# Kernel tuning notes

Hardware: AMD Instinct MI355X
Metric: run time of the kernel (lower is better)

The kernel has to match this reference:

```python
import jax, jax.numpy as jnp
import numpy as np
from jax import lax

NUM_CLUSTER = 128
N_ITERS = 10


def setup_inputs() -> dict:
    key = jax.random.key(0)
    feat_g = jax.random.normal(key, (131072, 256), dtype=jnp.float32)
    return {"feat_g": feat_g}


def _sq_dists(x, c):
    x2 = jnp.sum(x * x, axis=1, keepdims=True)            # [N,1]
    c2 = jnp.sum(c * c, axis=1)                           # [K]
    return x2 - 2.0 * (x @ c.T) + c2[None, :]


def _kmeans_fit(x, k, iters):
    n = x.shape[0]
    init_c = x[:k]  # deterministic init: first k points
    ones = jnp.ones((n,), dtype=x.dtype)

    def step(c, _):
        assign = jnp.argmin(_sq_dists(x, c), axis=1)                 # [N]
        sums = jax.ops.segment_sum(x, assign, num_segments=k)       # [K,d]
        counts = jax.ops.segment_sum(ones, assign, num_segments=k)  # [K]
        new_c = sums / jnp.maximum(counts, 1.0)[:, None]
        new_c = jnp.where(counts[:, None] > 0, new_c, c)  # keep empty clusters
        return new_c, None

    c, _ = lax.scan(step, init_c, None, length=iters)
    return c


def reference(feat_g):
    # view(batch, -1, dim) then view(-1, dim) is an identity reshape for the math
    x = lax.stop_gradient(feat_g)  # original detaches feat_gc before fit/predict
    c = _kmeans_fit(x, NUM_CLUSTER, N_ITERS)
    preds = jnp.argmin(_sq_dists(x, c), axis=1)  # [N] int labels
    return preds
```

## Files before the change

### kernel.cpp

```cpp
#include <hip/hip_runtime.h>

#define NPTS 131072
#define DIM 256
#define NK 128
#define NITER 10
#define SEG 16
#define SLICES 128
#define PTS_PER_SLICE (NPTS / SLICES)
#define CHUNK 128

typedef _Float16 half8 __attribute__((ext_vector_type(8)));
typedef _Float16 half4v __attribute__((ext_vector_type(4)));
typedef float f32x4 __attribute__((ext_vector_type(4)));

#define RSCALE 4096.0f
#define RINV 2.44140625e-4f

__global__ void x2_kernel(const float* __restrict__ x, float* __restrict__ x2) {
  int tid = threadIdx.x;
  int p = blockIdx.x * 16 + (tid >> 4);
  int part = tid & 15;
  const float4* xr = (const float4*)(x + (size_t)p * DIM);
  float s = 0.f;
#pragma unroll
  for (int j = 0; j < 4; ++j) {
    float4 v = xr[part * 4 + j];
    s += v.x * v.x;
    s += v.y * v.y;
    s += v.z * v.z;
    s += v.w * v.w;
  }
#pragma unroll
  for (int m = 8; m >= 1; m >>= 1) s += __shfl_xor(s, m, 16);
  if (part == 0) x2[p] = s;
}

__global__ void c2_kernel(const float* __restrict__ c, float* __restrict__ c2) {
  int k = blockIdx.x, lane = threadIdx.x;
  float4 v = ((const float4*)(c + (size_t)k * DIM))[lane];
  float s = v.x * v.x + v.y * v.y + v.z * v.z + v.w * v.w;
#pragma unroll
  for (int m = 32; m >= 1; m >>= 1) s += __shfl_xor(s, m, 64);
  if (lane == 0) c2[k] = s;
}

__global__ void convert_x2_kernel(const float* __restrict__ x, _Float16* __restrict__ x1,
                                  _Float16* __restrict__ x2s, float* __restrict__ x2) {
  int tid = threadIdx.x;
  int p = blockIdx.x * 16 + (tid >> 4);
  int part = tid & 15;
  const float4* xr = (const float4*)(x + (size_t)p * DIM);
  half8* o1 = (half8*)(x1 + (size_t)p * DIM);
  half8* o2 = (half8*)(x2s + (size_t)p * DIM);
  float s = 0.f;
  half8 hh[2], ll[2];
#pragma unroll
  for (int j = 0; j < 4; ++j) {
    float4 v = xr[part * 4 + j];
    float f[4] = {v.x, v.y, v.z, v.w};
#pragma unroll
    for (int u = 0; u < 4; ++u) {
      _Float16 hi = (_Float16)f[u];
      float r = f[u] - (float)hi;
      hh[j >> 1][(j & 1) * 4 + u] = hi;
      ll[j >> 1][(j & 1) * 4 + u] = (_Float16)(r * RSCALE);
      s += f[u] * f[u];
    }
  }
#pragma unroll
  for (int jj = 0; jj < 2; ++jj) {
    o1[part * 2 + jj] = hh[jj];
    o2[part * 2 + jj] = ll[jj];
  }
#pragma unroll
  for (int m = 8; m >= 1; m >>= 1) s += __shfl_xor(s, m, 16);
  if (part == 0) x2[p] = s;
}

__global__ void convert_c_kernel(const float* __restrict__ c, _Float16* __restrict__ ct) {
  int i = blockIdx.x * 256 + threadIdx.x;
  int k = i >> 6;
  int d4 = i & 63;
  float4 v = ((const float4*)c)[i];
  float f[4] = {v.x, v.y, v.z, v.w};
  half4v h, l;
#pragma unroll
  for (int j = 0; j < 4; ++j) {
    _Float16 hi = (_Float16)f[j];
    float r = f[j] - (float)hi;
    h[j] = hi;
    l[j] = (_Float16)(r * RSCALE);
  }
  int ch = d4 >> 3;
  int idx4 = ch * 2048 + k * 8 + (d4 & 7);
  ((half4v*)ct)[idx4] = h;
  ((half4v*)ct)[idx4 + 1024] = l;
}

template <bool DOHIST>
__global__ __launch_bounds__(256, 2) void assign_mfma_kernel(
    const _Float16* __restrict__ x1, const _Float16* __restrict__ x2s,
    const _Float16* __restrict__ ct, const float* __restrict__ x2,
    const float* __restrict__ c2, int* __restrict__ out, int* __restrict__ counts) {
  __shared__ __align__(16) _Float16 cbuf[2][8192];
  __shared__ int hcnt[NK];

  int tid = threadIdx.x;
  int lane = tid & 63;
  int w = tid >> 6;
  int lcol = lane & 15;
  int lgrp = lane >> 4;
  int row0 = blockIdx.x * 128 + w * 32;

  if (DOHIST && tid < NK) hcnt[tid] = 0;

  const _Float16* xa = x1 + (size_t)(row0 + lcol) * DIM + lgrp * 8;
  const _Float16* xb = x2s + (size_t)(row0 + lcol) * DIM + lgrp * 8;
  const half8* ctv = (const half8*)ct;

  f32x4 acc1[2][8], acc2[2][8];
#pragma unroll
  for (int rt = 0; rt < 2; ++rt)
#pragma unroll
    for (int c8 = 0; c8 < 8; ++c8) {
      acc1[rt][c8] = f32x4{0.f, 0.f, 0.f, 0.f};
      acc2[rt][c8] = f32x4{0.f, 0.f, 0.f, 0.f};
    }

  half8 A1[2], A2[2], nA1[2], nA2[2];

#pragma unroll
  for (int r = 0; r < 4; ++r) {
    __builtin_amdgcn_global_load_lds(
        (const __attribute__((address_space(1))) void*)(ctv + r * 256 + tid),
        (__attribute__((address_space(3))) void*)&((half8*)cbuf[0])[r * 256 + tid], 16, 0, 0);
  }
#pragma unroll
  for (int rt = 0; rt < 2; ++rt) {
    A1[rt] = *(const half8*)(xa + rt * 16 * DIM);
    A2[rt] = *(const half8*)(xb + rt * 16 * DIM);
  }
  __syncthreads();

#pragma unroll
  for (int ck = 0; ck < 8; ++ck) {
    const int cb = ck & 1;
    if (ck < 7) {
#pragma unroll
      for (int r = 0; r < 4; ++r) {
        __builtin_amdgcn_global_load_lds(
            (const __attribute__((address_space(1))) void*)(ctv + (ck + 1) * 1024 + r * 256 + tid),
            (__attribute__((address_space(3))) void*)&((half8*)cbuf[cb ^ 1])[r * 256 + tid], 16, 0,
            0);
      }
#pragma unroll
      for (int rt = 0; rt < 2; ++rt) {
        nA1[rt] = *(const half8*)(xa + rt * 16 * DIM + (ck + 1) * 32);
        nA2[rt] = *(const half8*)(xb + rt * 16 * DIM + (ck + 1) * 32);
      }
    }
#pragma unroll
    for (int c8 = 0; c8 < 8; ++c8) {
      int bidx = (c8 * 16 + lcol) * 32 + lgrp * 8;
      half8 b1 = *(const half8*)&cbuf[cb][bidx];
      half8 b2 = *(const half8*)&cbuf[cb][4096 + bidx];
#pragma unroll
      for (int rt = 0; rt < 2; ++rt) {
        acc1[rt][c8] = __builtin_amdgcn_mfma_f32_16x16x32_f16(A1[rt], b1, acc1[rt][c8], 0, 0, 0);
        acc2[rt][c8] = __builtin_amdgcn_mfma_f32_16x16x32_f16(A1[rt], b2, acc2[rt][c8], 0, 0, 0);
        acc2[rt][c8] = __builtin_amdgcn_mfma_f32_16x16x32_f16(A2[rt], b1, acc2[rt][c8], 0, 0, 0);
      }
    }
    if (ck < 7) {
#pragma unroll
      for (int rt = 0; rt < 2; ++rt) {
        A1[rt] = nA1[rt];
        A2[rt] = nA2[rt];
      }
      __syncthreads();
    }
  }

#pragma unroll
  for (int rt = 0; rt < 2; ++rt) {
    int pbase = row0 + rt * 16 + lgrp * 4;
    float x2p[4];
#pragma unroll
    for (int r = 0; r < 4; ++r) x2p[r] = x2[pbase + r];
    float bv[4];
    int bk[4];
#pragma unroll
    for (int r = 0; r < 4; ++r) { bv[r] = 3.4e38f; bk[r] = 0; }
#pragma unroll
    for (int c8 = 0; c8 < 8; ++c8) {
      int kc = c8 * 16 + lcol;
      float c2k = c2[kc];
#pragma unroll
      for (int r = 0; r < 4; ++r) {
        float dot = fmaf(acc2[rt][c8][r], RINV, acc1[rt][c8][r]);
        float d = fmaf(-2.f, dot, x2p[r]) + c2k;
        if (d < bv[r]) { bv[r] = d; bk[r] = kc; }
      }
    }
#pragma unroll
    for (int m = 1; m <= 8; m <<= 1) {
#pragma unroll
      for (int r = 0; r < 4; ++r) {
        float ov = __shfl_xor(bv[r], m, 64);
        int ok = __shfl_xor(bk[r], m, 64);
        if (ov < bv[r] || (ov == bv[r] && ok < bk[r])) { bv[r] = ov; bk[r] = ok; }
      }
    }
    if (lcol == 0) {
#pragma unroll
      for (int r = 0; r < 4; ++r) {
        out[pbase + r] = bk[r];
        if (DOHIST) atomicAdd(&hcnt[bk[r]], 1);
      }
    }
  }

  if (DOHIST) {
    __syncthreads();
    if (tid < NK) {
      int v = hcnt[tid];
      if (v) atomicAdd(&counts[tid], v);
    }
  }
}

__global__ __launch_bounds__(256, 4) void csum_kernel(
    const _Float16* __restrict__ x1, const _Float16* __restrict__ x2s,
    const int* __restrict__ assignb, float* __restrict__ p) {
  __shared__ __align__(16) _Float16 bt[2][2][32][136];
  __shared__ int abuf[2][CHUNK];

  int tid = threadIdx.x;
  int lane = tid & 63;
  int w = tid >> 6;
  int slice = blockIdx.x;
  int d0 = blockIdx.y * 32;
  int ibase = slice * PTS_PER_SLICE;
  int kbase = w * 32;
  int lcol = lane & 15;
  int lgrp = lane >> 4;

  int sarr = tid >> 7;
  int srow = tid & 127;
  const _Float16* xsrc = sarr ? x2s : x1;

  f32x4 acc1[2][2], acc2[2][2];
#pragma unroll
  for (int kt = 0; kt < 2; ++kt)
#pragma unroll
    for (int dt = 0; dt < 2; ++dt) {
      acc1[kt][dt] = f32x4{0.f, 0.f, 0.f, 0.f};
      acc2[kt][dt] = f32x4{0.f, 0.f, 0.f, 0.f};
    }

  {
    const half8* src = (const half8*)(xsrc + (size_t)(ibase + srow) * DIM + d0);
    half8 v[4];
#pragma unroll
    for (int q = 0; q < 4; ++q) v[q] = src[q];
#pragma unroll
    for (int q = 0; q < 4; ++q)
#pragma unroll
      for (int j = 0; j < 8; ++j) bt[0][sarr][q * 8 + j][srow] = v[q][j];
    if (tid < 32) ((int4*)abuf[0])[tid] = ((const int4*)(assignb + ibase))[tid];
  }
  __syncthreads();

  const int NCH = PTS_PER_SLICE / CHUNK;
  for (int ci = 0; ci < NCH; ++ci) {
    const int cb = ci & 1;
    half8 nv[4];
    int4 na;
    bool more = (ci < NCH - 1);
    if (more) {
      const half8* src =
          (const half8*)(xsrc + (size_t)(ibase + (ci + 1) * CHUNK + srow) * DIM + d0);
#pragma unroll
      for (int q = 0; q < 4; ++q) nv[q] = src[q];
      if (tid < 32) na = ((const int4*)(assignb + ibase + (ci + 1) * CHUNK))[tid];
    }

#pragma unroll
    for (int ks = 0; ks < 4; ++ks) {
      int4 av0 = ((int4*)abuf[cb])[ks * 8 + lgrp * 2];
      int4 av1 = ((int4*)abuf[cb])[ks * 8 + lgrp * 2 + 1];
      int aj[8] = {av0.x, av0.y, av0.z, av0.w, av1.x, av1.y, av1.z, av1.w};
      half8 oh[2];
#pragma unroll
      for (int kt = 0; kt < 2; ++kt) {
        int kk = kbase + kt * 16 + lcol;
#pragma unroll
        for (int j = 0; j < 8; ++j) oh[kt][j] = (aj[j] == kk) ? (_Float16)1.0f : (_Float16)0.0f;
      }
#pragma unroll
      for (int dt = 0; dt < 2; ++dt) {
        half8 b1 = *(const half8*)&bt[cb][0][dt * 16 + lcol][ks * 32 + lgrp * 8];
        half8 b2 = *(const half8*)&bt[cb][1][dt * 16 + lcol][ks * 32 + lgrp * 8];
#pragma unroll
        for (int kt = 0; kt < 2; ++kt) {
          acc1[kt][dt] = __builtin_amdgcn_mfma_f32_16x16x32_f16(oh[kt], b1, acc1[kt][dt], 0, 0, 0);
          acc2[kt][dt] = __builtin_amdgcn_mfma_f32_16x16x32_f16(oh[kt], b2, acc2[kt][dt], 0, 0, 0);
        }
      }
    }

    if (more) {
      __syncthreads();
#pragma unroll
      for (int q = 0; q < 4; ++q)
#pragma unroll
        for (int j = 0; j < 8; ++j) bt[cb ^ 1][sarr][q * 8 + j][srow] = nv[q][j];
      if (tid < 32) ((int4*)abuf[cb ^ 1])[tid] = na;
      __syncthreads();
    }
  }

#pragma unroll
  for (int kt = 0; kt < 2; ++kt)
#pragma unroll
    for (int dt = 0; dt < 2; ++dt) {
      int dd = d0 + dt * 16 + lcol;
#pragma unroll
      for (int r = 0; r < 4; ++r) {
        int krow = kbase + kt * 16 + lgrp * 4 + r;
        p[((size_t)slice * NK + krow) * DIM + dd] = fmaf(acc2[kt][dt][r], RINV, acc1[kt][dt][r]);
      }
    }
}

__global__ void reduce_v4_kernel(const float* __restrict__ p, int* __restrict__ counts,
                                 float* __restrict__ c, float* __restrict__ c2,
                                 _Float16* __restrict__ ct) {
  __shared__ float wsum[4];
  int k = blockIdx.x, d = threadIdx.x;
  int cnt = counts[k];
  float s = 0.f;
#pragma unroll 8
  for (int sl = 0; sl < SLICES; ++sl) s += p[((size_t)sl * NK + k) * DIM + d];

  float nc;
  if (cnt > 0)
    nc = s / fmaxf((float)cnt, 1.0f);
  else
    nc = c[(size_t)k * DIM + d];
  c[(size_t)k * DIM + d] = nc;

  {
    _Float16 hi = (_Float16)nc;
    float r = nc - (float)hi;
    _Float16 lov = (_Float16)(r * RSCALE);
    int ch = d >> 5, dd = d & 31;
    ct[ch * 8192 + k * 32 + dd] = hi;
    ct[ch * 8192 + k * 32 + dd + 4096] = lov;
  }

  float sq = nc * nc;
#pragma unroll
  for (int m = 32; m >= 1; m >>= 1) sq += __shfl_xor(sq, m, 64);
  if ((threadIdx.x & 63) == 0) wsum[threadIdx.x >> 6] = sq;
  __syncthreads();
  if (threadIdx.x == 0) {
    c2[k] = wsum[0] + wsum[1] + wsum[2] + wsum[3];
    counts[k] = 0;
  }
}

__global__ void assign_kernel(const float* __restrict__ x, const float* __restrict__ c,
                              const float* __restrict__ x2, const float* __restrict__ c2,
                              int* __restrict__ assign_out) {
  __shared__ float4 xs4[64 * 4];
  __shared__ float4 cs4[128 * 4];
  __shared__ float redv[64][17];
  __shared__ int redk[64][17];

  int tid = threadIdx.x;
  int tx = tid & 15;
  int ty = tid >> 4;
  int row0 = blockIdx.x * 64;

  float acc[4][8];
#pragma unroll
  for (int a = 0; a < 4; ++a)
#pragma unroll
    for (int b = 0; b < 8; ++b) acc[a][b] = 0.f;

  for (int ck = 0; ck < 16; ++ck) {
    {
      int p = tid >> 2, d4 = tid & 3;
      float4 v = *(const float4*)(x + (size_t)(row0 + p) * DIM + ck * 16 + d4 * 4);
      xs4[p * 4 + (d4 ^ ((p >> 2) & 3))] = v;
    }
#pragma unroll
    for (int r = 0; r < 2; ++r) {
      int idx = tid + r * 256;
      int kk = idx >> 2, dd = idx & 3;
      float4 v = *(const float4*)(c + (size_t)kk * DIM + ck * 16 + dd * 4);
      cs4[kk * 4 + (dd ^ ((kk >> 3) & 3))] = v;
    }
    __syncthreads();
#pragma unroll
    for (int d4 = 0; d4 < 4; ++d4) {
      float4 xr[4], cr[8];
#pragma unroll
      for (int pp = 0; pp < 4; ++pp) xr[pp] = xs4[(tx * 4 + pp) * 4 + (d4 ^ (tx & 3))];
#pragma unroll
      for (int kk = 0; kk < 8; ++kk) cr[kk] = cs4[(ty * 8 + kk) * 4 + (d4 ^ (ty & 3))];
#pragma unroll
      for (int pp = 0; pp < 4; ++pp)
#pragma unroll
        for (int kk = 0; kk < 8; ++kk) {
          acc[pp][kk] = fmaf(xr[pp].x, cr[kk].x, acc[pp][kk]);
          acc[pp][kk] = fmaf(xr[pp].y, cr[kk].y, acc[pp][kk]);
          acc[pp][kk] = fmaf(xr[pp].z, cr[kk].z, acc[pp][kk]);
          acc[pp][kk] = fmaf(xr[pp].w, cr[kk].w, acc[pp][kk]);
        }
    }
    __syncthreads();
  }

  float x2p[4];
#pragma unroll
  for (int pp = 0; pp < 4; ++pp) x2p[pp] = x2[row0 + tx * 4 + pp];

  float bestv[4];
  int bestk[4];
#pragma unroll
  for (int pp = 0; pp < 4; ++pp) { bestv[pp] = 3.4e38f; bestk[pp] = 0; }
#pragma unroll
  for (int kk = 0; kk < 8; ++kk) {
    float c2k = c2[ty * 8 + kk];
#pragma unroll
    for (int pp = 0; pp < 4; ++pp) {
      float d = fmaf(-2.f, acc[pp][kk], x2p[pp]) + c2k;
      if (d < bestv[pp]) { bestv[pp] = d; bestk[pp] = ty * 8 + kk; }
    }
  }
#pragma unroll
  for (int pp = 0; pp < 4; ++pp) {
    redv[tx * 4 + pp][ty] = bestv[pp];
    redk[tx * 4 + pp][ty] = bestk[pp];
  }
  __syncthreads();
  if (tid < 64) {
    float bv = redv[tid][0];
    int bk = redk[tid][0];
#pragma unroll
    for (int t = 1; t < 16; ++t) {
      float v = redv[tid][t];
      if (v < bv) { bv = v; bk = redk[tid][t]; }
    }
    assign_out[row0 + tid] = bk;
  }
}

__global__ void hist_kernel(const int* __restrict__ assign_in, int* __restrict__ hist) {
  __shared__ int h[NK];
  int tid = threadIdx.x, b = blockIdx.x;
  if (tid < NK) h[tid] = 0;
  __syncthreads();
#pragma unroll
  for (int r = 0; r < 4; ++r) {
    int a = assign_in[b * 1024 + r * 256 + tid];
    atomicAdd(&h[a], 1);
  }
  __syncthreads();
  if (tid < NK) hist[b * NK + tid] = h[tid];
}

__global__ void scan_fb_kernel(const int* __restrict__ hist, int* __restrict__ base,
                               int* __restrict__ counts, int* __restrict__ cbase) {
  __shared__ int h[128 * NK];
  int tid = threadIdx.x;
  for (int i = tid; i < 128 * NK; i += 256) h[i] = hist[i];
  __syncthreads();
  if (tid < NK) {
    int run = 0;
    for (int b = 0; b < 128; ++b) {
      int v = h[b * NK + tid];
      h[b * NK + tid] = run;
      run += v;
    }
    counts[tid] = run;
  }
  __syncthreads();
  if (tid == 0) {
    int cb = 0;
    for (int j = 0; j < NK; ++j) {
      cbase[j] = cb;
      cb += counts[j];
    }
  }
  __syncthreads();
  if (tid < NK) {
    int cbk = cbase[tid];
    for (int b = 0; b < 128; ++b) base[b * NK + tid] = h[b * NK + tid] + cbk;
  }
}

__global__ void scatter_kernel(const int* __restrict__ assign_in, const int* __restrict__ base,
                               int* __restrict__ perm) {
  __shared__ int cnt[NK];
  int lane = threadIdx.x, b = blockIdx.x;
  cnt[lane] = base[b * NK + lane];
  cnt[lane + 64] = base[b * NK + lane + 64];
  for (int r = 0; r < 16; ++r) {
    int p = b * 1024 + r * 64 + lane;
    int a = assign_in[p];
    unsigned long long mask = ~0ull;
#pragma unroll
    for (int j = 0; j < 7; ++j) {
      unsigned long long bal = __ballot((a >> j) & 1);
      mask &= ((a >> j) & 1) ? bal : ~bal;
    }
    int rank = __popcll(mask & ((1ull << lane) - 1ull));
    int pos = cnt[a] + rank;
    perm[pos] = p;
    if (rank == 0) cnt[a] += (int)__popcll(mask);
  }
}

__global__ void seg_sum_kernel(const float* __restrict__ x, const int* __restrict__ perm,
                               const int* __restrict__ counts, const int* __restrict__ cbase,
                               float* __restrict__ partial) {
  int k = blockIdx.x, s = blockIdx.y, d = threadIdx.x;
  int cnt = counts[k], off = cbase[k];
  int j0 = (int)(((long long)cnt * s) / SEG);
  int j1 = (int)(((long long)cnt * (s + 1)) / SEG);
  float sum = 0.f;
  int j = j0;
  for (; j + 4 <= j1; j += 4) {
    int p0 = perm[off + j + 0];
    int p1 = perm[off + j + 1];
    int p2 = perm[off + j + 2];
    int p3 = perm[off + j + 3];
    sum += x[(size_t)p0 * DIM + d];
    sum += x[(size_t)p1 * DIM + d];
    sum += x[(size_t)p2 * DIM + d];
    sum += x[(size_t)p3 * DIM + d];
  }
  for (; j < j1; ++j) sum += x[(size_t)perm[off + j] * DIM + d];
  partial[((size_t)k * SEG + s) * DIM + d] = sum;
}

__global__ void reduce_fb_kernel(const float* __restrict__ partial, const int* __restrict__ counts,
                                 float* __restrict__ c, float* __restrict__ c2) {
  __shared__ float wsum[4];
  int k = blockIdx.x, d = threadIdx.x;
  int cnt = counts[k];
  float s = 0.f;
#pragma unroll
  for (int t = 0; t < SEG; ++t) s += partial[((size_t)k * SEG + t) * DIM + d];
  float nc;
  if (cnt > 0)
    nc = s / fmaxf((float)cnt, 1.0f);
  else
    nc = c[(size_t)k * DIM + d];
  c[(size_t)k * DIM + d] = nc;
  float s2 = nc * nc;
#pragma unroll
  for (int m = 32; m >= 1; m >>= 1) s2 += __shfl_xor(s2, m, 64);
  if ((threadIdx.x & 63) == 0) wsum[threadIdx.x >> 6] = s2;
  __syncthreads();
  if (threadIdx.x == 0) c2[k] = wsum[0] + wsum[1] + wsum[2] + wsum[3];
}

extern "C" void kernel_launch(void* const* d_in, const int* in_sizes, int n_in,
                              void* d_out, int out_size, void* d_ws, size_t ws_size,
                              hipStream_t stream) {
  const float* x = (const float*)d_in[0];
  char* ws = (char*)d_ws;

  const size_t NEED_BIG = 152306688;
  bool use_mfma = ws_size >= NEED_BIG;

  if (use_mfma) {
    _Float16* x1 = (_Float16*)(ws + 0);
    _Float16* x2s = (_Float16*)(ws + 67108864);
    float* c = (float*)(ws + 134217728);
    _Float16* ct = (_Float16*)(ws + 134348800);
    float* c2 = (float*)(ws + 134479872);
    float* x2 = (float*)(ws + 134480384);
    int* assignb = (int*)(ws + 135004672);
    int* counts = (int*)(ws + 135528960);
    float* p = (float*)(ws + 135529472);

    hipMemcpyAsync(c, x, (size_t)NK * DIM * sizeof(float), hipMemcpyDeviceToDevice, stream);
    hipMemsetAsync(counts, 0, NK * sizeof(int), stream);
    convert_x2_kernel<<<NPTS / 16, 256, 0, stream>>>(x, x1, x2s, x2);
    c2_kernel<<<NK, 64, 0, stream>>>(c, c2);
    convert_c_kernel<<<NK * DIM / 4 / 256, 256, 0, stream>>>(c, ct);

    for (int it = 0; it < NITER; ++it) {
      assign_mfma_kernel<true>
          <<<NPTS / 128, 256, 0, stream>>>(x1, x2s, ct, x2, c2, assignb, counts);
      csum_kernel<<<dim3(SLICES, DIM / 32), 256, 0, stream>>>(x1, x2s, assignb, p);
      reduce_v4_kernel<<<NK, 256, 0, stream>>>(p, counts, c, c2, ct);
    }
    assign_mfma_kernel<false>
        <<<NPTS / 128, 256, 0, stream>>>(x1, x2s, ct, x2, c2, (int*)d_out, counts);
  } else {
    float* c = (float*)(ws + 0);
    float* c2 = (float*)(ws + 131072);
    float* x2 = (float*)(ws + 132096);
    int* assignb = (int*)(ws + 656384);
    int* hist = (int*)(ws + 1180672);
    int* base = (int*)(ws + 1246208);
    int* counts = (int*)(ws + 1311744);
    int* cbase = (int*)(ws + 1312256);
    int* perm = (int*)(ws + 1312768);
    float* partial = (float*)(ws + 1837056);

    hipMemcpyAsync(c, x, (size_t)NK * DIM * sizeof(float), hipMemcpyDeviceToDevice, stream);
    x2_kernel<<<NPTS / 16, 256, 0, stream>>>(x, x2);
    c2_kernel<<<NK, 64, 0, stream>>>(c, c2);

    for (int it = 0; it < NITER; ++it) {
      assign_kernel<<<NPTS / 64, 256, 0, stream>>>(x, c, x2, c2, assignb);
      hist_kernel<<<NPTS / 1024, 256, 0, stream>>>(assignb, hist);
      scan_fb_kernel<<<1, 256, 0, stream>>>(hist, base, counts, cbase);
      scatter_kernel<<<NPTS / 1024, 64, 0, stream>>>(assignb, base, perm);
      seg_sum_kernel<<<dim3(NK, SEG), 256, 0, stream>>>(x, perm, counts, cbase, partial);
      reduce_fb_kernel<<<NK, 256, 0, stream>>>(partial, counts, c, c2);
    }
    assign_kernel<<<NPTS / 64, 256, 0, stream>>>(x, c, x2, c2, (int*)d_out);
  }
}
```

Before: 982.1 us.

## Pre-transpose fp16 point data for csum and fuse conversion kernels

Adds a one-time conversion kernel that, besides producing the split fp16 hi/lo arrays and point norms, writes a transposed, tiled copy of the points (dimension-major per 128-point chunk) and also produces the initial centroid tiles and their norms from the first block. The per-iteration centroid-sum kernel then loads contiguous half8 vectors straight into its shared tile instead of doing a scalar transpose on every chunk of every iteration. The cost being removed is the repeated per-element shared-memory transpose in the hot loop; in exchange the workspace requirement roughly doubles (an extra ~140MB buffer) and the setup kernel does more work. If the workspace is smaller than the new threshold, the code falls back to the slow path.

```diff
diff --git a/kernel.cpp b/kernel.cpp
--- a/kernel.cpp
+++ b/kernel.cpp
@@ -44,57 +44,70 @@
   if (lane == 0) c2[k] = s;
 }
 
-__global__ void convert_x2_kernel(const float* __restrict__ x, _Float16* __restrict__ x1,
-                                  _Float16* __restrict__ x2s, float* __restrict__ x2) {
+__global__ __launch_bounds__(256) void convert_all_kernel(
+    const float* __restrict__ x, _Float16* __restrict__ x1, _Float16* __restrict__ x2s,
+    _Float16* __restrict__ xTp, float* __restrict__ x2, _Float16* __restrict__ ct,
+    float* __restrict__ c2) {
+  __shared__ _Float16 hbuf[2][128][33];
   int tid = threadIdx.x;
-  int p = blockIdx.x * 16 + (tid >> 4);
-  int part = tid & 15;
-  const float4* xr = (const float4*)(x + (size_t)p * DIM);
-  half8* o1 = (half8*)(x1 + (size_t)p * DIM);
-  half8* o2 = (half8*)(x2s + (size_t)p * DIM);
+  int b = blockIdx.x;
+  int ptl = tid >> 1, h = tid & 1;
+  size_t pt = (size_t)b * 128 + ptl;
   float s = 0.f;
-  half8 hh[2], ll[2];
-#pragma unroll
-  for (int j = 0; j < 4; ++j) {
-    float4 v = xr[part * 4 + j];
-    float f[4] = {v.x, v.y, v.z, v.w};
-#pragma unroll
-    for (int u = 0; u < 4; ++u) {
-      _Float16 hi = (_Float16)f[u];
-      float r = f[u] - (float)hi;
-      hh[j >> 1][(j & 1) * 4 + u] = hi;
-      ll[j >> 1][(j & 1) * 4 + u] = (_Float16)(r * RSCALE);
-      s += f[u] * f[u];
-    }
-  }
-#pragma unroll
-  for (int jj = 0; jj < 2; ++jj) {
-    o1[part * 2 + jj] = hh[jj];
-    o2[part * 2 + jj] = ll[jj];
-  }
-#pragma unroll
-  for (int m = 8; m >= 1; m >>= 1) s += __shfl_xor(s, m, 16);
-  if (part == 0) x2[p] = s;
-}
-
-__global__ void convert_c_kernel(const float* __restrict__ c, _Float16* __restrict__ ct) {
-  int i = blockIdx.x * 256 + threadIdx.x;
-  int k = i >> 6;
-  int d4 = i & 63;
-  float4 v = ((const float4*)c)[i];
-  float f[4] = {v.x, v.y, v.z, v.w};
-  half4v h, l;
-#pragma unroll
-  for (int j = 0; j < 4; ++j) {
-    _Float16 hi = (_Float16)f[j];
-    float r = f[j] - (float)hi;
-    h[j] = hi;
-    l[j] = (_Float16)(r * RSCALE);
-  }
-  int ch = d4 >> 3;
-  int idx4 = ch * 2048 + k * 8 + (d4 & 7);
-  ((half4v*)ct)[idx4] = h;
-  ((half4v*)ct)[idx4 + 1024] = l;
+  half8* xt8 = (half8*)xTp;
+
+  for (int dc = 0; dc < 8; ++dc) {
+    const float4* src = (const float4*)(x + pt * DIM + dc * 32 + h * 16);
+    half8 hh[2], ll[2];
+#pragma unroll
+    for (int q = 0; q < 4; ++q) {
+      float4 v = src[q];
+      float f[4] = {v.x, v.y, v.z, v.w};
+#pragma unroll
+      for (int u = 0; u < 4; ++u) {
+        _Float16 hi = (_Float16)f[u];
+        float r = f[u] - (float)hi;
+        hh[q >> 1][(q & 1) * 4 + u] = hi;
+        ll[q >> 1][(q & 1) * 4 + u] = (_Float16)(r * RSCALE);
+        s += f[u] * f[u];
+      }
+    }
+    half8* o1 = (half8*)(x1 + pt * DIM + dc * 32 + h * 16);
+    half8* o2 = (half8*)(x2s + pt * DIM + dc * 32 + h * 16);
+    o1[0] = hh[0];
+    o1[1] = hh[1];
+    o2[0] = ll[0];
+    o2[1] = ll[1];
+    if (b == 0) {
+#pragma unroll
+      for (int j = 0; j < 16; ++j) {
+        int d = h * 16 + j;
+        ct[dc * 8192 + ptl * 32 + d] = hh[j >> 3][j & 7];
+        ct[dc * 8192 + ptl * 32 + d + 4096] = ll[j >> 3][j & 7];
+      }
+    }
+    __syncthreads();
+#pragma unroll
+    for (int j = 0; j < 16; ++j) {
+      hbuf[0][ptl][h * 16 + j] = hh[j >> 3][j & 7];
+      hbuf[1][ptl][h * 16 + j] = ll[j >> 3][j & 7];
+    }
+    __syncthreads();
+#pragma unroll
+    for (int q = 0; q < 4; ++q) {
+      int o = q * 256 + tid;
+      int arr = o >> 9, d = (o >> 4) & 31, seg = o & 15;
+      half8 v;
+#pragma unroll
+      for (int j = 0; j < 8; ++j) v[j] = hbuf[arr][seg * 8 + j][d];
+      xt8[(size_t)((b * 8 + dc) * 2 + arr) * 544 + d * 17 + seg] = v;
+    }
+  }
+  float full = s + __shfl_xor(s, 1, 64);
+  if (h == 0) {
+    x2[pt] = full;
+    if (b == 0) c2[ptl] = full;
+  }
 }
 
 template <bool DOHIST>
@@ -229,9 +242,9 @@
   }
 }
 
-__global__ __launch_bounds__(256, 4) void csum_kernel(
-    const _Float16* __restrict__ x1, const _Float16* __restrict__ x2s,
-    const int* __restrict__ assignb, float* __restrict__ p) {
+__global__ __launch_bounds__(256, 4) void csum_kernel(const _Float16* __restrict__ xTp,
+                                                      const int* __restrict__ assignb,
+                                                      float* __restrict__ p) {
   __shared__ __align__(16) _Float16 bt[2][2][32][136];
   __shared__ int abuf[2][CHUNK];
 
@@ -239,15 +252,14 @@
   int lane = tid & 63;
   int w = tid >> 6;
   int slice = blockIdx.x;
-  int d0 = blockIdx.y * 32;
+  int dc = blockIdx.y;
+  int d0 = dc * 32;
   int ibase = slice * PTS_PER_SLICE;
   int kbase = w * 32;
   int lcol = lane & 15;
   int lgrp = lane >> 4;
 
-  int sarr = tid >> 7;
-  int srow = tid & 127;
-  const _Float16* xsrc = sarr ? x2s : x1;
+  const half8* xt8 = (const half8*)xTp;
 
   f32x4 acc1[2][2], acc2[2][2];
 #pragma unroll
@@ -259,14 +271,14 @@
     }
 
   {
-    const half8* src = (const half8*)(xsrc + (size_t)(ibase + srow) * DIM + d0);
-    half8 v[4];
-#pragma unroll
-    for (int q = 0; q < 4; ++q) v[q] = src[q];
-#pragma unroll
-    for (int q = 0; q < 4; ++q)
-#pragma unroll
-      for (int j = 0; j < 8; ++j) bt[0][sarr][q * 8 + j][srow] = v[q][j];
+    size_t tb = (size_t)((slice * 8 + 0) * 8 + dc) * 2 * 544;
+#pragma unroll
+    for (int q = 0; q < 4; ++q) {
+      int o = q * 256 + tid;
+      int arr = o >> 9, d = (o >> 4) & 31, seg = o & 15;
+      half8 v = xt8[tb + (size_t)arr * 544 + d * 17 + seg];
+      *(half8*)&bt[0][arr][d][seg * 8] = v;
+    }
     if (tid < 32) ((int4*)abuf[0])[tid] = ((const int4*)(assignb + ibase))[tid];
   }
   __syncthreads();
@@ -278,10 +290,13 @@
     int4 na;
     bool more = (ci < NCH - 1);
     if (more) {
-      const half8* src =
-          (const half8*)(xsrc + (size_t)(ibase + (ci + 1) * CHUNK + srow) * DIM + d0);
-#pragma unroll
-      for (int q = 0; q < 4; ++q) nv[q] = src[q];
+      size_t tb = (size_t)((slice * 8 + ci + 1) * 8 + dc) * 2 * 544;
+#pragma unroll
+      for (int q = 0; q < 4; ++q) {
+        int o = q * 256 + tid;
+        int arr = o >> 9, d = (o >> 4) & 31, seg = o & 15;
+        nv[q] = xt8[tb + (size_t)arr * 544 + d * 17 + seg];
+      }
       if (tid < 32) na = ((const int4*)(assignb + ibase + (ci + 1) * CHUNK))[tid];
     }
 
@@ -312,9 +327,11 @@
     if (more) {
       __syncthreads();
 #pragma unroll
-      for (int q = 0; q < 4; ++q)
-#pragma unroll
-        for (int j = 0; j < 8; ++j) bt[cb ^ 1][sarr][q * 8 + j][srow] = nv[q][j];
+      for (int q = 0; q < 4; ++q) {
+        int o = q * 256 + tid;
+        int arr = o >> 9, d = (o >> 4) & 31, seg = o & 15;
+        *(half8*)&bt[cb ^ 1][arr][d][seg * 8] = nv[q];
+      }
       if (tid < 32) ((int4*)abuf[cb ^ 1])[tid] = na;
       __syncthreads();
     }
@@ -575,7 +592,7 @@
   const float* x = (const float*)d_in[0];
   char* ws = (char*)d_ws;
 
-  const size_t NEED_BIG = 152306688;
+  const size_t NEED_BIG = 294913024;
   bool use_mfma = ws_size >= NEED_BIG;
 
   if (use_mfma) {
@@ -588,17 +605,16 @@
     int* assignb = (int*)(ws + 135004672);
     int* counts = (int*)(ws + 135528960);
     float* p = (float*)(ws + 135529472);
+    _Float16* xTp = (_Float16*)(ws + 152306688);
 
     hipMemcpyAsync(c, x, (size_t)NK * DIM * sizeof(float), hipMemcpyDeviceToDevice, stream);
     hipMemsetAsync(counts, 0, NK * sizeof(int), stream);
-    convert_x2_kernel<<<NPTS / 16, 256, 0, stream>>>(x, x1, x2s, x2);
-    c2_kernel<<<NK, 64, 0, stream>>>(c, c2);
-    convert_c_kernel<<<NK * DIM / 4 / 256, 256, 0, stream>>>(c, ct);
+    convert_all_kernel<<<NPTS / 128, 256, 0, stream>>>(x, x1, x2s, xTp, x2, ct, c2);
 
     for (int it = 0; it < NITER; ++it) {
       assign_mfma_kernel<true>
           <<<NPTS / 128, 256, 0, stream>>>(x1, x2s, ct, x2, c2, assignb, counts);
-      csum_kernel<<<dim3(SLICES, DIM / 32), 256, 0, stream>>>(x1, x2s, assignb, p);
+      csum_kernel<<<dim3(SLICES, DIM / 32), 256, 0, stream>>>(xTp, assignb, p);
       reduce_v4_kernel<<<NK, 256, 0, stream>>>(p, counts, c, c2, ct);
     }
     assign_mfma_kernel<false>
```

Result: slower. 1.019 ms (+3.8%).
